# Kernel optimization log

Measured on AMD Instinct MI355X. Metric: run time of the kernel, lower is better.

## Reference

```python
import jax, jax.numpy as jnp
import numpy as np


def setup_inputs() -> dict:
    key = jax.random.key(0)
    k1, k2, k3, k4, k5 = jax.random.split(key, 5)
    N, IN, OUT = 4096, 2048, 2048
    return {
        "input": jax.random.normal(k1, (N, IN), dtype=jnp.float32),
        "weight_mu": jax.random.normal(k2, (OUT, IN), dtype=jnp.float32) * 0.25,
        "weight_rho": jax.random.normal(k3, (OUT, IN), dtype=jnp.float32) - 5.0,
        "eps_weight": jax.random.normal(k4, (OUT, IN), dtype=jnp.float32),
        "bias": jax.random.normal(k5, (OUT,), dtype=jnp.float32) * 0.02,
    }


def reference(input, weight_mu, weight_rho, eps_weight, bias):
    # Effective weight: mu + softplus(rho) * eps   (log1p(exp(rho)) == softplus)
    w = weight_mu + jax.nn.softplus(weight_rho) * eps_weight  # [out, in]
    # F.linear: input @ w.T + bias
    return jnp.einsum("ni,oi->no", input, w) + bias
```

## Files before the change

kernel.cpp:

```cpp
#include <hip/hip_runtime.h>
#include <stdint.h>

typedef __bf16 bf16x8 __attribute__((ext_vector_type(8)));
typedef float f32x4 __attribute__((ext_vector_type(4)));
typedef float float4v __attribute__((ext_vector_type(4)));
typedef unsigned short u16x8 __attribute__((ext_vector_type(8)));

__device__ __forceinline__ unsigned short f2bf(float f) {
    unsigned u = __float_as_uint(f);
    u += 0x7fffu + ((u >> 16) & 1u);
    return (unsigned short)(u >> 16);
}

__device__ __forceinline__ float softplus(float x) {
    return fmaxf(x, 0.0f) + __logf(1.0f + __expf(-fabsf(x)));
}

__device__ __forceinline__ void gl_lds16(const void* gptr, void* lptr) {
    auto g = reinterpret_cast<const __attribute__((address_space(1))) void*>(
        reinterpret_cast<uintptr_t>(gptr));
    auto l = reinterpret_cast<__attribute__((address_space(3))) void*>(
        reinterpret_cast<uintptr_t>(lptr));
    __builtin_amdgcn_global_load_lds(g, l, 16, 0, 0);
}

__global__ void prep_kernel(const float* __restrict__ in,
                            const float* __restrict__ mu,
                            const float* __restrict__ rho,
                            const float* __restrict__ eps,
                            unsigned short* __restrict__ in_bf,
                            unsigned short* __restrict__ w_bf,
                            int nIn8, int nW8) {
    int i = blockIdx.x * blockDim.x + threadIdx.x;
    if (i < nIn8) {
        const float4v* p = (const float4v*)in + (size_t)i * 2;
        float4v a = p[0], b = p[1];
        u16x8 r;
        r[0] = f2bf(a[0]); r[1] = f2bf(a[1]); r[2] = f2bf(a[2]); r[3] = f2bf(a[3]);
        r[4] = f2bf(b[0]); r[5] = f2bf(b[1]); r[6] = f2bf(b[2]); r[7] = f2bf(b[3]);
        ((u16x8*)in_bf)[i] = r;
    } else {
        int j = i - nIn8;
        if (j >= nW8) return;
        const float4v* pm = (const float4v*)mu  + (size_t)j * 2;
        const float4v* pr = (const float4v*)rho + (size_t)j * 2;
        const float4v* pe = (const float4v*)eps + (size_t)j * 2;
        float4v m0 = pm[0], m1 = pm[1];
        float4v r0 = pr[0], r1 = pr[1];
        float4v e0 = pe[0], e1 = pe[1];
        u16x8 r;
        r[0] = f2bf(m0[0] + softplus(r0[0]) * e0[0]);
        r[1] = f2bf(m0[1] + softplus(r0[1]) * e0[1]);
        r[2] = f2bf(m0[2] + softplus(r0[2]) * e0[2]);
        r[3] = f2bf(m0[3] + softplus(r0[3]) * e0[3]);
        r[4] = f2bf(m1[0] + softplus(r1[0]) * e1[0]);
        r[5] = f2bf(m1[1] + softplus(r1[1]) * e1[1]);
        r[6] = f2bf(m1[2] + softplus(r1[2]) * e1[2]);
        r[7] = f2bf(m1[3] + softplus(r1[3]) * e1[3]);
        ((u16x8*)w_bf)[j] = r;
    }
}

#define BM 128
#define BN 128
#define BK 64

__global__ __launch_bounds__(512, 4)
void gemm_bt_kernel(const unsigned short* __restrict__ A,
                    const unsigned short* __restrict__ B,
                    const float* __restrict__ bias,
                    float* __restrict__ C,
                    int M, int N, int K) {
    __shared__ unsigned short lds_a[2][BM * BK];
    __shared__ unsigned short lds_b[2][BN * BK];

    const int t      = threadIdx.x;
    const int lane   = t & 63;
    const int wave   = t >> 6;
    const int lane16 = lane & 15;
    const int quad   = lane >> 4;
    const int wm     = wave & 1;
    const int wn     = wave >> 1;

    const int m0 = blockIdx.y * BM;
    const int n0 = blockIdx.x * BN;

    const int r1   = t >> 3;
    const int pkg1 = t & 7;
    const int g1   = (pkg1 ^ (r1 & 7)) * 8;
    const int r2   = r1 + 64;
    const int g2   = (pkg1 ^ (r2 & 7)) * 8;

    const unsigned short* Ab = A + (size_t)m0 * K;
    const unsigned short* Bb = B + (size_t)n0 * K;

    f32x4 acc[4][2] = {};
    const int sw = lane16 & 7;

    auto stage = [&](int buf, int k0) {
        gl_lds16(Ab + (size_t)r1 * K + k0 + g1, &lds_a[buf][t * 8]);
        gl_lds16(Ab + (size_t)r2 * K + k0 + g2, &lds_a[buf][4096 + t * 8]);
        gl_lds16(Bb + (size_t)r1 * K + k0 + g1, &lds_b[buf][t * 8]);
        gl_lds16(Bb + (size_t)r2 * K + k0 + g2, &lds_b[buf][4096 + t * 8]);
    };

    const int nit = K / BK;
    stage(0, 0);
    __syncthreads();

    auto body = [&](int cur, int it) {
        const unsigned short* la = lds_a[cur];
        const unsigned short* lb = lds_b[cur];
        bf16x8 af[2][4], bfr[2][2];
#pragma unroll
        for (int ch = 0; ch < 2; ch++) {
            const int pk = ((ch * 4 + quad) ^ sw) * 8;
#pragma unroll
            for (int mi = 0; mi < 4; mi++)
                af[ch][mi] = *(const bf16x8*)(la + (wm * 64 + mi * 16 + lane16) * BK + pk);
#pragma unroll
            for (int ni = 0; ni < 2; ni++)
                bfr[ch][ni] = *(const bf16x8*)(lb + (wn * 32 + ni * 16 + lane16) * BK + pk);
        }
        if (it + 1 < nit) stage(cur ^ 1, (it + 1) * BK);
#pragma unroll
        for (int ch = 0; ch < 2; ch++)
#pragma unroll
            for (int mi = 0; mi < 4; mi++)
#pragma unroll
                for (int ni = 0; ni < 2; ni++)
                    acc[mi][ni] = __builtin_amdgcn_mfma_f32_16x16x32_bf16(
                        af[ch][mi], bfr[ch][ni], acc[mi][ni], 0, 0, 0);
        __syncthreads();
    };

    for (int it = 0; it < nit; it += 2) {
        body(0, it);
        body(1, it + 1);
    }

    float bv[2];
#pragma unroll
    for (int ni = 0; ni < 2; ni++)
        bv[ni] = bias[n0 + wn * 32 + ni * 16 + lane16];

#pragma unroll
    for (int mi = 0; mi < 4; mi++) {
        const int rbase = m0 + wm * 64 + mi * 16 + quad * 4;
#pragma unroll
        for (int ni = 0; ni < 2; ni++) {
            const int col = n0 + wn * 32 + ni * 16 + lane16;
#pragma unroll
            for (int r = 0; r < 4; r++)
                C[(size_t)(rbase + r) * N + col] = acc[mi][ni][r] + bv[ni];
        }
    }
}

extern "C" void kernel_launch(void* const* d_in, const int* in_sizes, int n_in,
                              void* d_out, int out_size, void* d_ws, size_t ws_size,
                              hipStream_t stream) {
    const float* input = (const float*)d_in[0];
    const float* mu    = (const float*)d_in[1];
    const float* rho   = (const float*)d_in[2];
    const float* eps   = (const float*)d_in[3];
    const float* bias  = (const float*)d_in[4];
    float* out = (float*)d_out;

    const int OUT = in_sizes[4];
    const int IN  = in_sizes[1] / OUT;
    const int M   = in_sizes[0] / IN;

    unsigned short* in_bf = (unsigned short*)d_ws;
    unsigned short* w_bf  = in_bf + (size_t)M * IN;

    const int nIn8 = (M * IN) / 8;
    const int nW8  = (OUT * IN) / 8;
    prep_kernel<<<dim3((nIn8 + nW8 + 255) / 256), 256, 0, stream>>>(
        input, mu, rho, eps, in_bf, w_bf, nIn8, nW8);

    gemm_bt_kernel<<<dim3(OUT / BN, M / BM), 512, 0, stream>>>(
        in_bf, w_bf, bias, out, M, OUT, IN);
}
```

Baseline: 159.9 us.

## Stage GEMM tiles through registers with single LDS buffer and smaller N tile

Replaces the direct global-to-LDS async loads and double-buffered LDS with register prefetch: the next K-tile is loaded into registers while MFMAs run on the current LDS tile, then written to a single LDS buffer between two barriers. The block tile shrinks from 128x128 with 512 threads to 128x64 with 256 threads, halving LDS use and doubling the grid. This aims for more resident blocks and simpler scheduling, but adds a second barrier per iteration, more register pressure and more global traffic per output because of the smaller N tile.

```diff
diff --git a/kernel.cpp b/kernel.cpp
--- a/kernel.cpp
+++ b/kernel.cpp
@@ -5,6 +5,7 @@
 typedef float f32x4 __attribute__((ext_vector_type(4)));
 typedef float float4v __attribute__((ext_vector_type(4)));
 typedef unsigned short u16x8 __attribute__((ext_vector_type(8)));
+typedef unsigned int u32x4 __attribute__((ext_vector_type(4)));
 
 __device__ __forceinline__ unsigned short f2bf(float f) {
     unsigned u = __float_as_uint(f);
@@ -14,14 +15,6 @@
 
 __device__ __forceinline__ float softplus(float x) {
     return fmaxf(x, 0.0f) + __logf(1.0f + __expf(-fabsf(x)));
-}
-
-__device__ __forceinline__ void gl_lds16(const void* gptr, void* lptr) {
-    auto g = reinterpret_cast<const __attribute__((address_space(1))) void*>(
-        reinterpret_cast<uintptr_t>(gptr));
-    auto l = reinterpret_cast<__attribute__((address_space(3))) void*>(
-        reinterpret_cast<uintptr_t>(lptr));
-    __builtin_amdgcn_global_load_lds(g, l, 16, 0, 0);
 }
 
 __global__ void prep_kernel(const float* __restrict__ in,
@@ -62,17 +55,17 @@
 }
 
 #define BM 128
-#define BN 128
+#define BN 64
 #define BK 64
 
-__global__ __launch_bounds__(512, 4)
+__global__ __launch_bounds__(256, 4)
 void gemm_bt_kernel(const unsigned short* __restrict__ A,
                     const unsigned short* __restrict__ B,
                     const float* __restrict__ bias,
                     float* __restrict__ C,
                     int M, int N, int K) {
-    __shared__ unsigned short lds_a[2][BM * BK];
-    __shared__ unsigned short lds_b[2][BN * BK];
+    __shared__ unsigned short lds_a[BM * BK];
+    __shared__ unsigned short lds_b[BN * BK];
 
     const int t      = threadIdx.x;
     const int lane   = t & 63;
@@ -85,44 +78,64 @@
     const int m0 = blockIdx.y * BM;
     const int n0 = blockIdx.x * BN;
 
-    const int r1   = t >> 3;
-    const int pkg1 = t & 7;
-    const int g1   = (pkg1 ^ (r1 & 7)) * 8;
-    const int r2   = r1 + 64;
-    const int g2   = (pkg1 ^ (r2 & 7)) * 8;
+    const int pkg = t & 7;
+    int arow[4], ago[4];
+#pragma unroll
+    for (int j = 0; j < 4; j++) {
+        arow[j] = (j * 256 + t) >> 3;
+        ago[j]  = (pkg ^ (arow[j] & 7)) * 8;
+    }
+    int brow[2], bgo[2];
+#pragma unroll
+    for (int j = 0; j < 2; j++) {
+        brow[j] = (j * 256 + t) >> 3;
+        bgo[j]  = (pkg ^ (brow[j] & 7)) * 8;
+    }
 
     const unsigned short* Ab = A + (size_t)m0 * K;
     const unsigned short* Bb = B + (size_t)n0 * K;
 
+    u32x4 ra[4], rb[2];
+    auto load6 = [&](int k0) {
+#pragma unroll
+        for (int j = 0; j < 4; j++)
+            ra[j] = *(const u32x4*)(Ab + (size_t)arow[j] * K + k0 + ago[j]);
+#pragma unroll
+        for (int j = 0; j < 2; j++)
+            rb[j] = *(const u32x4*)(Bb + (size_t)brow[j] * K + k0 + bgo[j]);
+    };
+    auto write6 = [&]() {
+#pragma unroll
+        for (int j = 0; j < 4; j++)
+            *(u32x4*)(lds_a + (j * 256 + t) * 8) = ra[j];
+#pragma unroll
+        for (int j = 0; j < 2; j++)
+            *(u32x4*)(lds_b + (j * 256 + t) * 8) = rb[j];
+    };
+
     f32x4 acc[4][2] = {};
     const int sw = lane16 & 7;
+    const int nit = K / BK;
 
-    auto stage = [&](int buf, int k0) {
-        gl_lds16(Ab + (size_t)r1 * K + k0 + g1, &lds_a[buf][t * 8]);
-        gl_lds16(Ab + (size_t)r2 * K + k0 + g2, &lds_a[buf][4096 + t * 8]);
-        gl_lds16(Bb + (size_t)r1 * K + k0 + g1, &lds_b[buf][t * 8]);
-        gl_lds16(Bb + (size_t)r2 * K + k0 + g2, &lds_b[buf][4096 + t * 8]);
-    };
-
-    const int nit = K / BK;
-    stage(0, 0);
+    load6(0);
+    write6();
     __syncthreads();
 
-    auto body = [&](int cur, int it) {
-        const unsigned short* la = lds_a[cur];
-        const unsigned short* lb = lds_b[cur];
+    for (int it = 0; it < nit; it++) {
+        if (it + 1 < nit) load6((it + 1) * BK);
+
         bf16x8 af[2][4], bfr[2][2];
 #pragma unroll
         for (int ch = 0; ch < 2; ch++) {
             const int pk = ((ch * 4 + quad) ^ sw) * 8;
 #pragma unroll
             for (int mi = 0; mi < 4; mi++)
-                af[ch][mi] = *(const bf16x8*)(la + (wm * 64 + mi * 16 + lane16) * BK + pk);
+                af[ch][mi] = *(const bf16x8*)(lds_a + (wm * 64 + mi * 16 + lane16) * BK + pk);
 #pragma unroll
             for (int ni = 0; ni < 2; ni++)
-                bfr[ch][ni] = *(const bf16x8*)(lb + (wn * 32 + ni * 16 + lane16) * BK + pk);
+                bfr[ch][ni] = *(const bf16x8*)(lds_b + (wn * 32 + ni * 16 + lane16) * BK + pk);
         }
-        if (it + 1 < nit) stage(cur ^ 1, (it + 1) * BK);
+
 #pragma unroll
         for (int ch = 0; ch < 2; ch++)
 #pragma unroll
@@ -131,12 +144,12 @@
                 for (int ni = 0; ni < 2; ni++)
                     acc[mi][ni] = __builtin_amdgcn_mfma_f32_16x16x32_bf16(
                         af[ch][mi], bfr[ch][ni], acc[mi][ni], 0, 0, 0);
-        __syncthreads();
-    };
 
-    for (int it = 0; it < nit; it += 2) {
-        body(0, it);
-        body(1, it + 1);
+        if (it + 1 < nit) {
+            __syncthreads();
+            write6();
+            __syncthreads();
+        }
     }
 
     float bv[2];
@@ -179,6 +192,6 @@
     prep_kernel<<<dim3((nIn8 + nW8 + 255) / 256), 256, 0, stream>>>(
         input, mu, rho, eps, in_bf, w_bf, nIn8, nW8);
 
-    gemm_bt_kernel<<<dim3(OUT / BN, M / BM), 512, 0, stream>>>(
+    gemm_bt_kernel<<<dim3(OUT / BN, M / BM), 256, 0, stream>>>(
         in_bf, w_bf, bias, out, M, OUT, IN);
 }
```

Result: slower. 171.2 us (+7.0%).

## Load B fragments directly from global into registers, dropping B LDS staging

Applied to the files above, without the earlier changes.

The B (weight) tile is no longer staged through shared memory. Each wave loads its own B fragments straight from global memory into registers, double-buffered one iteration ahead, while A keeps the LDS double-buffer path. This halves LDS footprint and LDS read traffic, which could allow more occupancy. In exchange, global loads are redundant across the waves that share the same wn, and they are less coalesced (16-byte chunks spread across rows). It also adds register pressure and exposes global-load latency inside the loop.

```diff
diff --git a/kernel.cpp b/kernel.cpp
--- a/kernel.cpp
+++ b/kernel.cpp
@@ -72,7 +72,6 @@
                     float* __restrict__ C,
                     int M, int N, int K) {
     __shared__ unsigned short lds_a[2][BM * BK];
-    __shared__ unsigned short lds_b[2][BN * BK];
 
     const int t      = threadIdx.x;
     const int lane   = t & 63;
@@ -86,43 +85,51 @@
     const int n0 = blockIdx.x * BN;
 
     const int r1   = t >> 3;
-    const int pkg1 = t & 7;
-    const int g1   = (pkg1 ^ (r1 & 7)) * 8;
+    const int pkg  = t & 7;
+    const int g1   = (pkg ^ (r1 & 7)) * 8;
     const int r2   = r1 + 64;
-    const int g2   = (pkg1 ^ (r2 & 7)) * 8;
+    const int g2   = (pkg ^ (r2 & 7)) * 8;
 
     const unsigned short* Ab = A + (size_t)m0 * K;
-    const unsigned short* Bb = B + (size_t)n0 * K;
+
+    const unsigned short* pB0 =
+        B + (size_t)(n0 + wn * 32 + lane16) * K + quad * 8;
+    const unsigned short* pB1 = pB0 + (size_t)16 * K;
 
     f32x4 acc[4][2] = {};
-    const int sw = lane16 & 7;
+    const int sw  = lane16 & 7;
+    const int nit = K / BK;
 
-    auto stage = [&](int buf, int k0) {
+    auto stageA = [&](int buf, int k0) {
         gl_lds16(Ab + (size_t)r1 * K + k0 + g1, &lds_a[buf][t * 8]);
         gl_lds16(Ab + (size_t)r2 * K + k0 + g2, &lds_a[buf][4096 + t * 8]);
-        gl_lds16(Bb + (size_t)r1 * K + k0 + g1, &lds_b[buf][t * 8]);
-        gl_lds16(Bb + (size_t)r2 * K + k0 + g2, &lds_b[buf][4096 + t * 8]);
+    };
+    auto loadB = [&](bf16x8 (&dst)[2][2], int k0) {
+#pragma unroll
+        for (int ch = 0; ch < 2; ch++) {
+            dst[ch][0] = *(const bf16x8*)(pB0 + k0 + ch * 32);
+            dst[ch][1] = *(const bf16x8*)(pB1 + k0 + ch * 32);
+        }
     };
 
-    const int nit = K / BK;
-    stage(0, 0);
+    bf16x8 bX[2][2], bY[2][2];
+
+    loadB(bX, 0);
+    stageA(0, 0);
     __syncthreads();
 
-    auto body = [&](int cur, int it) {
-        const unsigned short* la = lds_a[cur];
-        const unsigned short* lb = lds_b[cur];
-        bf16x8 af[2][4], bfr[2][2];
+    auto body = [&](int cur, int it, bf16x8 (&bcur)[2][2], bf16x8 (&bnxt)[2][2]) {
+        if (it + 1 < nit) loadB(bnxt, (it + 1) * BK);
+        bf16x8 af[2][4];
 #pragma unroll
         for (int ch = 0; ch < 2; ch++) {
             const int pk = ((ch * 4 + quad) ^ sw) * 8;
 #pragma unroll
             for (int mi = 0; mi < 4; mi++)
-                af[ch][mi] = *(const bf16x8*)(la + (wm * 64 + mi * 16 + lane16) * BK + pk);
-#pragma unroll
-            for (int ni = 0; ni < 2; ni++)
-                bfr[ch][ni] = *(const bf16x8*)(lb + (wn * 32 + ni * 16 + lane16) * BK + pk);
+                af[ch][mi] = *(const bf16x8*)(&lds_a[cur][0] +
+                               (wm * 64 + mi * 16 + lane16) * BK + pk);
         }
-        if (it + 1 < nit) stage(cur ^ 1, (it + 1) * BK);
+        if (it + 1 < nit) stageA(cur ^ 1, (it + 1) * BK);
 #pragma unroll
         for (int ch = 0; ch < 2; ch++)
 #pragma unroll
@@ -130,13 +137,13 @@
 #pragma unroll
                 for (int ni = 0; ni < 2; ni++)
                     acc[mi][ni] = __builtin_amdgcn_mfma_f32_16x16x32_bf16(
-                        af[ch][mi], bfr[ch][ni], acc[mi][ni], 0, 0, 0);
+                        af[ch][mi], bcur[ch][ni], acc[mi][ni], 0, 0, 0);
         __syncthreads();
     };
 
     for (int it = 0; it < nit; it += 2) {
-        body(0, it);
-        body(1, it + 1);
+        body(0, it,     bX, bY);
+        body(1, it + 1, bY, bX);
     }
 
     float bv[2];
```

Measured after the change: 197.0 us. +23.2%, slower.
